# Kernel optimization log

Measured on AMD Instinct MI355X. Metric: run time of the kernel, lower is better.

## Reference

```python
import jax, jax.numpy as jnp
import numpy as np
import math

SUPPORT = 4
NEI = 20
POOL_RATE = 4

def _normalize(x, axis):
    n = jnp.linalg.norm(x, axis=axis, keepdims=True)
    return x / jnp.maximum(n, 1e-12)

def _knn(verts, k):
    # verts: (b, v, 3) -> (b, v, k) indices of k nearest (excluding self)
    sq = jnp.sum(verts * verts, axis=-1)
    dist = sq[:, :, None] + sq[:, None, :] - 2.0 * jnp.einsum('bid,bjd->bij', verts, verts)
    _, idx = jax.lax.top_k(-dist, k + 1)
    return idx[:, :, 1:]

def _gather(t, idx):
    # t: (b, v, c), idx: (b, v, n) -> (b, v, n, c)
    return jax.vmap(lambda ti, ii: ti[ii])(t, idx)

def _conv_surface(idx, verts, dirs, support, kernel):
    b, v, n = idx.shape
    nd = _normalize(_gather(verts, idx) - verts[:, :, None, :], -1)  # (b,v,n,3)
    sd = _normalize(dirs, 0)                                          # (3, s*k)
    theta = jax.nn.relu(jnp.einsum('bvnd,de->bvne', nd, sd))
    theta = theta.reshape(b, v, n, support, kernel)
    return jnp.sum(jnp.max(theta, axis=2), axis=2)  # (b, v, kernel)

def _conv_layer(idx, verts, fm, W, bias, dirs, support, out_c):
    b, v, n = idx.shape
    nd = _normalize(_gather(verts, idx) - verts[:, :, None, :], -1)
    sd = _normalize(dirs, 0)                                          # (3, s*out)
    theta = jax.nn.relu(jnp.einsum('bvnd,de->bvne', nd, sd))          # (b,v,n,s*out)
    f = jnp.einsum('bvc,ce->bve', fm, W) + bias                       # (b,v,(s+1)*out)
    f_center = f[:, :, :out_c]
    f_support = _gather(f[:, :, out_c:], idx)                         # (b,v,n,s*out)
    act = (theta * f_support).reshape(b, v, n, support, out_c)
    return f_center + jnp.sum(jnp.max(act, axis=2), axis=2)

def _pool(verts, fm, idx, key, rate):
    pooled = jnp.max(_gather(fm, idx), axis=2)  # (b, v, c)
    v = verts.shape[1]
    sel = jax.random.permutation(key, v)[: v // rate]
    return verts[:, sel, :], pooled[:, sel, :]

def _unif(key, shape, stdv):
    return jax.random.uniform(key, shape, jnp.float32, -stdv, stdv)

def setup_inputs() -> dict:
    key = jax.random.key(0)
    ks = jax.random.split(key, 16)
    s = SUPPORT
    vertices = jax.random.normal(ks[0], (4, 1, 4096, 3), dtype=jnp.float32)
    d = {'vertices': vertices}
    d['dirs0'] = _unif(ks[1], (3, s * 32), 1.0 / math.sqrt(s * 32))
    layers = [(32, 64), (64, 128), (128, 256), (256, 1024)]
    for i, (cin, cout) in enumerate(layers, start=1):
        stdv = 1.0 / math.sqrt(cout * (s + 1))
        d[f'W{i}'] = _unif(ks[3 * i - 1], (cin, (s + 1) * cout), stdv)
        d[f'b{i}'] = _unif(ks[3 * i], ((s + 1) * cout,), stdv)
        d[f'D{i}'] = _unif(ks[3 * i + 1], (3, s * cout), stdv)
    return d

def reference(vertices, dirs0, W1, b1, D1, W2, b2, D2, W3, b3, D3, W4, b4, D4):
    s = SUPPORT
    bs, _, vn, _ = vertices.shape
    v = vertices.reshape(bs, vn, 3)
    idx = _knn(v, NEI)
    fm0 = jax.nn.relu(_conv_surface(idx, v, dirs0, s, 32))
    fm1 = jax.nn.relu(_conv_layer(idx, v, fm0, W1, b1, D1, s, 64))
    v, fm1 = _pool(v, fm1, idx, jax.random.key(42), POOL_RATE)
    idx = _knn(v, NEI)
    fm2 = jax.nn.relu(_conv_layer(idx, v, fm1, W2, b2, D2, s, 128))
    fm3 = jax.nn.relu(_conv_layer(idx, v, fm2, W3, b3, D3, s, 256))
    v, fm3 = _pool(v, fm3, idx, jax.random.key(43), POOL_RATE)
    idx = _knn(v, NEI)
    fm4 = _conv_layer(idx, v, fm3, W4, b4, D4, s, 1024)
    out = jnp.transpose(fm4, (0, 2, 1))[..., None]  # (bs, 1024, vn/16, 1)
    return out
```

## Files before the change

### kernel.cpp

```cpp
#include <hip/hip_runtime.h>
#include <vector>
#include <algorithm>
#include <cstdint>
#include <cstring>
#include <cmath>

static inline uint32_t tf_rotl(uint32_t x, int r) { return (x << r) | (x >> (32 - r)); }

static void tf2x32(uint32_t k0, uint32_t k1, uint32_t x0, uint32_t x1,
                   uint32_t* o0, uint32_t* o1) {
  uint32_t ks2 = k0 ^ k1 ^ 0x1BD11BDAu;
  uint32_t v0 = x0 + k0, v1 = x1 + k1;
  static const int R0[4] = {13, 15, 26, 6}, R1[4] = {17, 29, 16, 24};
#define RND4(R) do { for (int i_ = 0; i_ < 4; ++i_) { v0 += v1; v1 = tf_rotl(v1, R[i_]); v1 ^= v0; } } while (0)
  RND4(R0); v0 += k1;  v1 += ks2 + 1u;
  RND4(R1); v0 += ks2; v1 += k0 + 2u;
  RND4(R0); v0 += k0;  v1 += k1 + 3u;
  RND4(R1); v0 += k1;  v1 += ks2 + 4u;
  RND4(R0); v0 += ks2; v1 += k0 + 5u;
#undef RND4
  *o0 = v0; *o1 = v1;
}

static void jax_permutation(uint32_t seed, int n, int rounds, int* x) {
  uint32_t k0 = 0u, k1 = seed;
  for (int i = 0; i < n; ++i) x[i] = i;
  std::vector<uint32_t> bits(n);
  std::vector<int> ord(n), xn(n);
  for (int r = 0; r < rounds; ++r) {
    uint32_t nk0, nk1, sk0, sk1;
    tf2x32(k0, k1, 0u, 0u, &nk0, &nk1);
    tf2x32(k0, k1, 0u, 1u, &sk0, &sk1);
    for (int i = 0; i < n; ++i) {
      uint32_t h, l;
      tf2x32(sk0, sk1, 0u, (uint32_t)i, &h, &l);
      bits[i] = h ^ l;
    }
    for (int i = 0; i < n; ++i) ord[i] = i;
    std::stable_sort(ord.begin(), ord.end(),
                     [&](int a, int b) { return bits[a] < bits[b]; });
    for (int i = 0; i < n; ++i) xn[i] = x[ord[i]];
    memcpy(x, xn.data(), (size_t)n * sizeof(int));
    k0 = nk0; k1 = nk1;
  }
}

#define NEI 20

__device__ __forceinline__ float san(float v) {
  v = (v != v) ? 0.0f : v;
  return fmaxf(-1e4f, fminf(v, 1e4f));
}

__global__ void k_setup(const float* __restrict__ vin, float* __restrict__ outA,
                        float4* __restrict__ pk, int nverts,
                        const float* __restrict__ d0, const float* __restrict__ d1,
                        const float* __restrict__ d2, const float* __restrict__ d3,
                        const float* __restrict__ d4,
                        float* __restrict__ s0, float* __restrict__ s1,
                        float* __restrict__ s2, float* __restrict__ s3,
                        float* __restrict__ s4) {
  int blk = blockIdx.x;
  if (blk < 64) {
    int i = blk * 256 + threadIdx.x;
    if (i >= nverts) return;
    float x = san(vin[3 * i]), y = san(vin[3 * i + 1]), z = san(vin[3 * i + 2]);
    outA[3 * i] = x; outA[3 * i + 1] = y; outA[3 * i + 2] = z;
    pk[i] = make_float4(x, y, z, x * x + y * y + z * z);
    return;
  }
  int t = (blk - 64) * 256 + threadIdx.x;
  const float* d; float* s; int E, e;
  if (t < 128)       { d = d0; s = s0; E = 128;  e = t; }
  else if (t < 384)  { d = d1; s = s1; E = 256;  e = t - 128; }
  else if (t < 896)  { d = d2; s = s2; E = 512;  e = t - 384; }
  else if (t < 1920) { d = d3; s = s3; E = 1024; e = t - 896; }
  else if (t < 6016) { d = d4; s = s4; E = 4096; e = t - 1920; }
  else return;
  float a = san(d[e]);
  float b = san(d[E + e]);
  float c = san(d[2 * E + e]);
  float nrm = sqrtf(a * a + b * b + c * c);
  float m = fmaxf(nrm, 1e-12f);
  s[e] = a / m; s[E + e] = b / m; s[2 * E + e] = c / m;
}

__device__ __forceinline__ unsigned fmap(float f) {
  unsigned u = __float_as_uint(f);
  return u ^ ((u & 0x80000000u) ? 0xFFFFFFFFu : 0x80000000u);
}

__device__ __forceinline__ unsigned dpp_min_bcast1(unsigned a) {
  unsigned t;
  t = (unsigned)__builtin_amdgcn_update_dpp((int)a, (int)a, 0xB1, 0xF, 0xF, true);
  a = t < a ? t : a;
  t = (unsigned)__builtin_amdgcn_update_dpp((int)a, (int)a, 0x4E, 0xF, 0xF, true);
  a = t < a ? t : a;
  t = (unsigned)__builtin_amdgcn_update_dpp((int)a, (int)a, 0x141, 0xF, 0xF, true);
  a = t < a ? t : a;
  t = (unsigned)__builtin_amdgcn_update_dpp((int)a, (int)a, 0x140, 0xF, 0xF, true);
  a = t < a ? t : a;
  t = (unsigned)__builtin_amdgcn_update_dpp((int)a, (int)a, 0x142, 0xA, 0xF, false);
  a = t < a ? t : a;
  t = (unsigned)__builtin_amdgcn_update_dpp((int)a, (int)a, 0x143, 0xC, 0xF, false);
  a = t < a ? t : a;
  return (unsigned)__builtin_amdgcn_readlane((int)a, 63);
}

__device__ __forceinline__ void dpp_min_bcast2(unsigned& a, unsigned& b) {
  unsigned t0, t1;
#define STEP_DPP(ctrl, rm, bc)                                                           \
  t0 = (unsigned)__builtin_amdgcn_update_dpp((int)a, (int)a, ctrl, rm, 0xF, bc);         \
  t1 = (unsigned)__builtin_amdgcn_update_dpp((int)b, (int)b, ctrl, rm, 0xF, bc);         \
  a = t0 < a ? t0 : a; b = t1 < b ? t1 : b;
  STEP_DPP(0xB1, 0xF, true)
  STEP_DPP(0x4E, 0xF, true)
  STEP_DPP(0x141, 0xF, true)
  STEP_DPP(0x140, 0xF, true)
  STEP_DPP(0x142, 0xA, false)
  STEP_DPP(0x143, 0xC, false)
#undef STEP_DPP
  a = (unsigned)__builtin_amdgcn_readlane((int)a, 63);
  b = (unsigned)__builtin_amdgcn_readlane((int)b, 63);
}

template <int VCAND>
__global__ __launch_bounds__(256, 8) void k_knn8(const float4* __restrict__ pk,
                                                 int* __restrict__ nidx, int V) {
  const int wid = threadIdx.x >> 6;
  const int lane = threadIdx.x & 63;
  const int row0 = blockIdx.x * 8 + wid * 2;
  const int b = row0 / V;
  const int base = b * V;
  const int i0 = row0 % V;

  float xi[2], yi[2], zi[2], sqi[2];
#pragma unroll
  for (int t = 0; t < 2; ++t) {
    float4 q = pk[base + i0 + t];
    xi[t] = q.x; yi[t] = q.y; zi[t] = q.z; sqi[t] = q.w;
  }

  unsigned long long q0[2] = {~0ULL, ~0ULL}, q1[2] = {~0ULL, ~0ULL}, q2[2] = {~0ULL, ~0ULL};
#pragma unroll 4
  for (int c = 0; c < VCAND; ++c) {
    int j = c * 64 + lane;
    float4 cj = pk[base + j];
    float xj = cj.x, yj = cj.y, zj = cj.z, sqj = cj.w;
#pragma unroll
    for (int t = 0; t < 2; ++t) {
      float dot = xi[t] * xj + yi[t] * yj + zi[t] * zj;
      float dd = (sqi[t] + sqj) - 2.0f * dot;
      unsigned long long k = (((unsigned long long)fmap(dd)) << 32) | (unsigned)j;
      if (k < q2[t]) {
        if (k < q1[t]) {
          q2[t] = q1[t];
          if (k < q0[t]) { q1[t] = q0[t]; q0[t] = k; } else { q1[t] = k; }
        } else {
          q2[t] = k;
        }
      }
    }
  }

  for (int r = 0; r < 21; ++r) {
    unsigned h0 = (unsigned)(q0[0] >> 32);
    unsigned h1 = (unsigned)(q0[1] >> 32);
    unsigned m0 = h0, m1 = h1;
    dpp_min_bcast2(m0, m1);
    unsigned long long mk0 = __ballot(h0 == m0);
    unsigned long long mk1 = __ballot(h1 == m1);
    bool win0, win1;
    if (__popcll(mk0) > 1) {
      unsigned jj = (h0 == m0) ? (unsigned)q0[0] : 0xFFFFFFFFu;
      unsigned jm = dpp_min_bcast1(jj);
      win0 = (h0 == m0) && ((unsigned)q0[0] == jm);
    } else {
      win0 = (h0 == m0);
    }
    if (__popcll(mk1) > 1) {
      unsigned jj = (h1 == m1) ? (unsigned)q0[1] : 0xFFFFFFFFu;
      unsigned jm = dpp_min_bcast1(jj);
      win1 = (h1 == m1) && ((unsigned)q0[1] == jm);
    } else {
      win1 = (h1 == m1);
    }
    if (win0) {
      if (r > 0) nidx[(size_t)row0 * NEI + (r - 1)] = (int)(unsigned)q0[0];
      unsigned long long bound = q0[0];
      q0[0] = q1[0]; q1[0] = q2[0]; q2[0] = ~0ULL;
      if (q0[0] == ~0ULL) {
        unsigned long long nm = ~0ULL;
        for (int c = 0; c < VCAND; ++c) {
          int j = c * 64 + lane;
          float4 cj = pk[base + j];
          float dot = xi[0] * cj.x + yi[0] * cj.y + zi[0] * cj.z;
          float dd = (sqi[0] + cj.w) - 2.0f * dot;
          unsigned long long k = (((unsigned long long)fmap(dd)) << 32) | (unsigned)j;
          if (k > bound && k < nm) nm = k;
        }
        q0[0] = nm;
      }
    }
    if (win1) {
      if (r > 0) nidx[(size_t)(row0 + 1) * NEI + (r - 1)] = (int)(unsigned)q0[1];
      unsigned long long bound = q0[1];
      q0[1] = q1[1]; q1[1] = q2[1]; q2[1] = ~0ULL;
      if (q0[1] == ~0ULL) {
        unsigned long long nm = ~0ULL;
        for (int c = 0; c < VCAND; ++c) {
          int j = c * 64 + lane;
          float4 cj = pk[base + j];
          float dot = xi[1] * cj.x + yi[1] * cj.y + zi[1] * cj.z;
          float dd = (sqi[1] + cj.w) - 2.0f * dot;
          unsigned long long k = (((unsigned long long)fmap(dd)) << 32) | (unsigned)j;
          if (k > bound && k < nm) nm = k;
        }
        q0[1] = nm;
      }
    }
  }
}

__global__ __launch_bounds__(128) void k_conv_surface(const float* __restrict__ verts,
                                                      const int* __restrict__ nidx,
                                                      const float* __restrict__ sd,
                                                      float* __restrict__ fm, int V) {
  int row = blockIdx.x;
  int b = row / V, v = row % V;
  const float* vb = verts + (size_t)b * V * 3;
  __shared__ float nd[60];
  __shared__ float mcol[128];
  int tid = threadIdx.x;
  if (tid < NEI) {
    int j = nidx[(size_t)row * NEI + tid];
    float dx = vb[3 * j] - vb[3 * v];
    float dy = vb[3 * j + 1] - vb[3 * v + 1];
    float dz = vb[3 * j + 2] - vb[3 * v + 2];
    float nrm = sqrtf(dx * dx + dy * dy + dz * dz);
    float m = fmaxf(nrm, 1e-12f);
    nd[tid * 3] = dx / m; nd[tid * 3 + 1] = dy / m; nd[tid * 3 + 2] = dz / m;
  }
  __syncthreads();
  {
    int e = tid;
    float s0 = sd[e], s1 = sd[128 + e], s2 = sd[256 + e];
    float me = 0.0f;
#pragma unroll
    for (int n = 0; n < NEI; ++n) {
      float th = nd[3 * n] * s0 + nd[3 * n + 1] * s1 + nd[3 * n + 2] * s2;
      th = fmaxf(th, 0.0f);
      me = fmaxf(me, th);
    }
    mcol[e] = me;
  }
  __syncthreads();
  if (tid < 32) {
    float o = mcol[tid] + mcol[32 + tid] + mcol[64 + tid] + mcol[96 + tid];
    o = fmaxf(o, 0.0f);
    fm[(size_t)row * 32 + tid] = o;
  }
}

__global__ __launch_bounds__(256) void k_gemm_bias(const float* __restrict__ A,
                                                   const float* __restrict__ W,
                                                   const float* __restrict__ bias,
                                                   float* __restrict__ Cm,
                                                   int M, int N, int K) {
  __shared__ float As[16][68];
  __shared__ float Bs[16][68];
  int n0 = blockIdx.x * 64, m0 = blockIdx.y * 64;
  int tx = threadIdx.x & 15, ty = threadIdx.x >> 4;
  float acc[4][4] = {};
  for (int k0 = 0; k0 < K; k0 += 16) {
    for (int t = threadIdx.x; t < 1024; t += 256) {
      int mm = t >> 4, kk = t & 15;
      int m = m0 + mm;
      As[kk][mm] = (m < M) ? A[(size_t)m * K + (k0 + kk)] : 0.0f;
    }
    for (int t = threadIdx.x; t < 1024; t += 256) {
      int kk = t >> 6, nn = t & 63;
      int n = n0 + nn;
      Bs[kk][nn] = (n < N) ? san(W[(size_t)(k0 + kk) * N + n]) : 0.0f;
    }
    __syncthreads();
#pragma unroll
    for (int kk = 0; kk < 16; ++kk) {
      float4 av = *(const float4*)&As[kk][ty << 2];
      float4 bv = *(const float4*)&Bs[kk][tx << 2];
      float a[4] = {av.x, av.y, av.z, av.w};
      float bb[4] = {bv.x, bv.y, bv.z, bv.w};
#pragma unroll
      for (int i = 0; i < 4; ++i)
#pragma unroll
        for (int j = 0; j < 4; ++j) acc[i][j] += a[i] * bb[j];
    }
    __syncthreads();
  }
  for (int i = 0; i < 4; ++i)
    for (int j = 0; j < 4; ++j) {
      int m = m0 + (ty << 2) + i, n = n0 + (tx << 2) + j;
      if (m < M && n < N) Cm[(size_t)m * N + n] = acc[i][j] + san(bias[n]);
    }
}

__global__ __launch_bounds__(256) void k_gemm128(const float* __restrict__ A,
                                                 const float* __restrict__ W,
                                                 const float* __restrict__ bias,
                                                 float* __restrict__ Cm,
                                                 int M, int N, int K) {
  __shared__ float As[32][132];
  __shared__ float Bs[32][132];
  const int n0 = blockIdx.x * 128, m0 = blockIdx.y * 128;
  const int tx = threadIdx.x & 15, ty = threadIdx.x >> 4;
  const int bm = ty * 8;
  float acc[8][8] = {};
  float bias_lo[4], bias_hi[4];
#pragma unroll
  for (int j = 0; j < 4; ++j) {
    bias_lo[j] = san(bias[n0 + tx * 4 + j]);
    bias_hi[j] = san(bias[n0 + 64 + tx * 4 + j]);
  }
  for (int k0 = 0; k0 < K; k0 += 32) {
#pragma unroll
    for (int r = 0; r < 4; ++r) {
      int t = r * 256 + threadIdx.x;
      int mm = t >> 3, kk = (t & 7) * 4;
      float4 v = *(const float4*)&A[(size_t)(m0 + mm) * K + k0 + kk];
      As[kk + 0][mm] = v.x; As[kk + 1][mm] = v.y; As[kk + 2][mm] = v.z; As[kk + 3][mm] = v.w;
    }
#pragma unroll
    for (int r = 0; r < 4; ++r) {
      int t = r * 256 + threadIdx.x;
      int kk = t >> 5, nn = (t & 31) * 4;
      float4 v = *(const float4*)&W[(size_t)(k0 + kk) * N + n0 + nn];
      *(float4*)&Bs[kk][nn] = v;
    }
    __syncthreads();
#pragma unroll
    for (int kk = 0; kk < 32; ++kk) {
      float4 a0 = *(const float4*)&As[kk][bm];
      float4 a1 = *(const float4*)&As[kk][bm + 4];
      float4 b0 = *(const float4*)&Bs[kk][tx * 4];
      float4 b1 = *(const float4*)&Bs[kk][64 + tx * 4];
      float a[8] = {a0.x, a0.y, a0.z, a0.w, a1.x, a1.y, a1.z, a1.w};
      float bb[8] = {b0.x, b0.y, b0.z, b0.w, b1.x, b1.y, b1.z, b1.w};
#pragma unroll
      for (int i = 0; i < 8; ++i)
#pragma unroll
        for (int j = 0; j < 8; ++j) acc[i][j] += a[i] * bb[j];
    }
    __syncthreads();
  }
#pragma unroll
  for (int i = 0; i < 8; ++i) {
    int m = m0 + bm + i;
    float4 lo = {acc[i][0] + bias_lo[0], acc[i][1] + bias_lo[1],
                 acc[i][2] + bias_lo[2], acc[i][3] + bias_lo[3]};
    float4 hi = {acc[i][4] + bias_hi[0], acc[i][5] + bias_hi[1],
                 acc[i][6] + bias_hi[2], acc[i][7] + bias_hi[3]};
    *(float4*)&Cm[(size_t)m * N + n0 + tx * 4] = lo;
    *(float4*)&Cm[(size_t)m * N + n0 + 64 + tx * 4] = hi;
  }
}

__global__ __launch_bounds__(256) void k_conv_layer(const float* __restrict__ f,
                                                    const float* __restrict__ verts,
                                                    const int* __restrict__ nidx,
                                                    const float* __restrict__ sd,
                                                    float* __restrict__ outf,
                                                    int V, int C, int relu_out) {
  int row = blockIdx.x;
  int b = row / V, v = row % V;
  int E = 4 * C;
  extern __shared__ float sm[];
  float* mcol = sm;
  float* nd = sm + E;
  int* jr = (int*)(nd + 60);
  int tid = threadIdx.x;
  const float* vb = verts + (size_t)b * V * 3;
  if (tid < NEI) {
    int j = nidx[(size_t)row * NEI + tid];
    jr[tid] = j;
    float dx = vb[3 * j] - vb[3 * v];
    float dy = vb[3 * j + 1] - vb[3 * v + 1];
    float dz = vb[3 * j + 2] - vb[3 * v + 2];
    float nrm = sqrtf(dx * dx + dy * dy + dz * dz);
    float m = fmaxf(nrm, 1e-12f);
    nd[tid * 3] = dx / m; nd[tid * 3 + 1] = dy / m; nd[tid * 3 + 2] = dz / m;
  }
  __syncthreads();
  size_t fb = (size_t)b * V;
  int fivec = 5 * C;
  for (int e = tid; e < E; e += blockDim.x) {
    float s0 = sd[e], s1 = sd[E + e], s2 = sd[2 * E + e];
    float me = -INFINITY;
#pragma unroll
    for (int n = 0; n < NEI; ++n) {
      float th = nd[3 * n] * s0 + nd[3 * n + 1] * s1 + nd[3 * n + 2] * s2;
      th = fmaxf(th, 0.0f);
      float fv = f[(fb + jr[n]) * (size_t)fivec + C + e];
      me = fmaxf(me, th * fv);
    }
    mcol[e] = me;
  }
  __syncthreads();
  for (int c = tid; c < C; c += blockDim.x) {
    float o = f[(size_t)row * fivec + c] + mcol[c] + mcol[C + c] + mcol[2 * C + c] + mcol[3 * C + c];
    if (relu_out) o = fmaxf(o, 0.0f);
    outf[(size_t)row * C + c] = o;
  }
}

__global__ __launch_bounds__(1024) void k_conv_layer_big(const float* __restrict__ f,
                                                         const float* __restrict__ verts,
                                                         const int* __restrict__ nidx,
                                                         const float* __restrict__ sd,
                                                         float* __restrict__ outf,
                                                         int V, int C, int relu_out) {
  int row = blockIdx.x;
  int b = row / V, v = row % V;
  int E = 4 * C;
  extern __shared__ float sm[];
  float* mcol = sm;
  float* nd = sm + E;
  int* jr = (int*)(nd + 60);
  int tid = threadIdx.x;
  const float* vb = verts + (size_t)b * V * 3;
  if (tid < NEI) {
    int j = nidx[(size_t)row * NEI + tid];
    jr[tid] = j;
    float dx = vb[3 * j] - vb[3 * v];
    float dy = vb[3 * j + 1] - vb[3 * v + 1];
    float dz = vb[3 * j + 2] - vb[3 * v + 2];
    float nrm = sqrtf(dx * dx + dy * dy + dz * dz);
    float m = fmaxf(nrm, 1e-12f);
    nd[tid * 3] = dx / m; nd[tid * 3 + 1] = dy / m; nd[tid * 3 + 2] = dz / m;
  }
  __syncthreads();
  size_t fb = (size_t)b * V;
  int fivec = 5 * C;
  for (int e = tid; e < E; e += blockDim.x) {
    float s0 = sd[e], s1 = sd[E + e], s2 = sd[2 * E + e];
    float me = -INFINITY;
#pragma unroll
    for (int n = 0; n < NEI; ++n) {
      float th = nd[3 * n] * s0 + nd[3 * n + 1] * s1 + nd[3 * n + 2] * s2;
      th = fmaxf(th, 0.0f);
      float fv = f[(fb + jr[n]) * (size_t)fivec + C + e];
      me = fmaxf(me, th * fv);
    }
    mcol[e] = me;
  }
  __syncthreads();
  for (int c = tid; c < C; c += blockDim.x) {
    float o = f[(size_t)row * fivec + c] + mcol[c] + mcol[C + c] + mcol[2 * C + c] + mcol[3 * C + c];
    if (relu_out) o = fmaxf(o, 0.0f);
    outf[(size_t)row * C + c] = o;
  }
}

__global__ __launch_bounds__(256) void k_transpose_vc(const float* __restrict__ in,
                                                      float* __restrict__ out,
                                                      int V, int C) {
  __shared__ float tile[32][33];
  int b = blockIdx.z;
  int c0 = blockIdx.x * 32, v0 = blockIdx.y * 32;
  int tx = threadIdx.x & 31, ty4 = threadIdx.x >> 5;
#pragma unroll
  for (int j = 0; j < 4; ++j) {
    int v = v0 + ty4 * 4 + j;
    tile[ty4 * 4 + j][tx] = in[((size_t)b * V + v) * C + c0 + tx];
  }
  __syncthreads();
#pragma unroll
  for (int j = 0; j < 4; ++j) {
    int c = c0 + ty4 * 4 + j;
    out[((size_t)b * C + c) * V + v0 + tx] = tile[tx][ty4 * 4 + j];
  }
}

__global__ void k_pool_sel(const float* __restrict__ fm, const int* __restrict__ nidx,
                           const int* __restrict__ sel, float* __restrict__ outp,
                           const float* __restrict__ vinA, float* __restrict__ voutA,
                           float4* __restrict__ pkout,
                           int Vin, int Vout, int C) {
  int t = blockIdx.x * blockDim.x + threadIdx.x;
  if (t < 4 * Vout) {
    int p = t % Vout;
    int b = t / Vout;
    int src = b * Vin + sel[p];
    float x = vinA[3 * src], y = vinA[3 * src + 1], z = vinA[3 * src + 2];
    int dst = b * Vout + p;
    voutA[3 * dst] = x; voutA[3 * dst + 1] = y; voutA[3 * dst + 2] = z;
    pkout[dst] = make_float4(x, y, z, x * x + y * y + z * z);
  }
  int total = 4 * Vout * C;
  if (t >= total) return;
  int c = t % C;
  int p = (t / C) % Vout;
  int b = t / (C * Vout);
  int sv = sel[p];
  const int* ir = nidx + ((size_t)b * Vin + sv) * NEI;
  float m = -INFINITY;
#pragma unroll
  for (int n = 0; n < NEI; ++n)
    m = fmaxf(m, fm[((size_t)b * Vin + ir[n]) * C + c]);
  outp[((size_t)b * Vout + p) * C + c] = m;
}

extern "C" void kernel_launch(void* const* d_in, const int* in_sizes, int n_in,
                              void* d_out, int out_size, void* d_ws, size_t ws_size,
                              hipStream_t stream) {
  (void)in_sizes; (void)n_in; (void)out_size; (void)ws_size;
  const int B = 4, V1 = 4096, V2 = 1024, V3 = 256;

  const float* vin   = (const float*)d_in[0];
  const float* dirs0 = (const float*)d_in[1];
  const float* W1 = (const float*)d_in[2];
  const float* b1 = (const float*)d_in[3];
  const float* D1 = (const float*)d_in[4];
  const float* W2 = (const float*)d_in[5];
  const float* b2 = (const float*)d_in[6];
  const float* D2 = (const float*)d_in[7];
  const float* W3 = (const float*)d_in[8];
  const float* b3 = (const float*)d_in[9];
  const float* D3 = (const float*)d_in[10];
  const float* W4 = (const float*)d_in[11];
  const float* b4 = (const float*)d_in[12];
  const float* D4 = (const float*)d_in[13];
  float* out = (float*)d_out;

  char* ws = (char*)d_ws;
  size_t off = 0;
  auto alloc = [&](size_t bytes) -> char* {
    char* p = ws + off;
    off = (off + bytes + 255) & ~(size_t)255;
    return p;
  };
  int* sel1 = (int*)alloc((size_t)V2 * 4);
  int* sel2 = (int*)alloc((size_t)V3 * 4);
  float* verts1 = (float*)alloc((size_t)B * V1 * 3 * 4);
  float* verts2 = (float*)alloc((size_t)B * V2 * 3 * 4);
  float* verts3 = (float*)alloc((size_t)B * V3 * 3 * 4);
  float4* pk1 = (float4*)alloc((size_t)B * V1 * 16);
  float4* pk2 = (float4*)alloc((size_t)B * V2 * 16);
  float4* pk3 = (float4*)alloc((size_t)B * V3 * 16);
  int* idx1 = (int*)alloc((size_t)B * V1 * NEI * 4);
  int* idx2 = (int*)alloc((size_t)B * V2 * NEI * 4);
  int* idx3 = (int*)alloc((size_t)B * V3 * NEI * 4);
  float* sd0 = (float*)alloc(3 * 128 * 4);
  float* sd1 = (float*)alloc(3 * 256 * 4);
  float* sd2 = (float*)alloc(3 * 512 * 4);
  float* sd3 = (float*)alloc(3 * 1024 * 4);
  float* sd4 = (float*)alloc(3 * 4096 * 4);
  float* bufA = (float*)alloc((size_t)B * V1 * 32 * 4);
  float* bufB = (float*)alloc((size_t)B * V1 * 64 * 4);
  float* bufC = (float*)alloc((size_t)B * V2 * 64 * 4);
  float* fbuf = (float*)alloc((size_t)B * V1 * 320 * 4);
  float* fm0 = bufA, *fm2 = bufA;
  float* fm1 = bufB, *fm3 = bufB;
  float* fm1p = bufC, *fm3p = bufC;
  float* conv4out = bufB;

  static int perm1[4096];
  static int perm2[1024];
  static int selh[1280];
  jax_permutation(42u, 4096, 2, perm1);
  jax_permutation(43u, 1024, 1, perm2);
  memcpy(selh, perm1, 1024 * sizeof(int));
  memcpy(selh + 1024, perm2, 256 * sizeof(int));
  hipMemcpyAsync(sel1, selh, 1024 * sizeof(int), hipMemcpyHostToDevice, stream);
  hipMemcpyAsync(sel2, selh + 1024, 256 * sizeof(int), hipMemcpyHostToDevice, stream);

  k_setup<<<88, 256, 0, stream>>>(vin, verts1, pk1, B * V1,
                                  dirs0, D1, D2, D3, D4, sd0, sd1, sd2, sd3, sd4);
  k_knn8<64><<<B * V1 / 8, 256, 0, stream>>>(pk1, idx1, V1);
  k_conv_surface<<<B * V1, 128, 0, stream>>>(verts1, idx1, sd0, fm0, V1);
  k_gemm_bias<<<dim3(5, 256), 256, 0, stream>>>(fm0, W1, b1, fbuf, B * V1, 320, 32);
  k_conv_layer<<<B * V1, 256, (4 * 64 + 80) * 4, stream>>>(fbuf, verts1, idx1, sd1, fm1, V1, 64, 1);
  {
    int total = B * V2 * 64;
    k_pool_sel<<<(total + 255) / 256, 256, 0, stream>>>(fm1, idx1, sel1, fm1p,
                                                        verts1, verts2, pk2,
                                                        V1, V2, 64);
  }
  k_knn8<16><<<B * V2 / 8, 256, 0, stream>>>(pk2, idx2, V2);
  k_gemm128<<<dim3(640 / 128, 4096 / 128), 256, 0, stream>>>(fm1p, W2, b2, fbuf, B * V2, 640, 64);
  k_conv_layer<<<B * V2, 256, (4 * 128 + 80) * 4, stream>>>(fbuf, verts2, idx2, sd2, fm2, V2, 128, 1);
  k_gemm128<<<dim3(1280 / 128, 4096 / 128), 256, 0, stream>>>(fm2, W3, b3, fbuf, B * V2, 1280, 128);
  k_conv_layer<<<B * V2, 256, (4 * 256 + 80) * 4, stream>>>(fbuf, verts2, idx2, sd3, fm3, V2, 256, 1);
  {
    int total = B * V3 * 256;
    k_pool_sel<<<(total + 255) / 256, 256, 0, stream>>>(fm3, idx2, sel2, fm3p,
                                                        verts2, verts3, pk3,
                                                        V2, V3, 256);
  }
  k_knn8<4><<<B * V3 / 8, 256, 0, stream>>>(pk3, idx3, V3);
  k_gemm128<<<dim3(5120 / 128, 1024 / 128), 256, 0, stream>>>(fm3p, W4, b4, fbuf, B * V3, 5120, 256);
  k_conv_layer_big<<<B * V3, 1024, (4 * 1024 + 80) * 4, stream>>>(fbuf, verts3, idx3, sd4, conv4out, V3, 1024, 0);
  k_transpose_vc<<<dim3(1024 / 32, 256 / 32, B), 256, 0, stream>>>(conv4out, out, V3, 1024);
}
```

Measured before the change: 439.3 us.

## Replace FP32 GEMMs with split-bf16 MFMA (3-term) matrix-core kernel

Replaces the scalar FP32 128x128 tiled GEMM used by layers 2-4 with a matrix-core kernel built on bf16 16x16x32 MFMA. Each operand is split into high and low bf16 parts, and three products (hh, hl, lh) approximate FP32 accuracy. Weights are split and transposed each call by new kernels, and activations are split before every GEMM. This moves the GEMM FLOPs onto matrix cores, at the cost of extra split kernels, extra memory traffic, and slightly lower precision than true FP32.

Result: faster. 403.2 us (-8.2%).

```diff
diff --git a/kernel.cpp b/kernel.cpp
--- a/kernel.cpp
+++ b/kernel.cpp
@@ -304,64 +304,113 @@
     }
 }
 
-__global__ __launch_bounds__(256) void k_gemm128(const float* __restrict__ A,
-                                                 const float* __restrict__ W,
-                                                 const float* __restrict__ bias,
-                                                 float* __restrict__ Cm,
-                                                 int M, int N, int K) {
-  __shared__ float As[32][132];
-  __shared__ float Bs[32][132];
+typedef __attribute__((ext_vector_type(8))) short v8h;
+typedef __attribute__((ext_vector_type(4))) float v4f;
+
+__device__ __forceinline__ unsigned short f2bf(float f) {
+  unsigned u = __float_as_uint(f);
+  u = u + 0x7FFFu + ((u >> 16) & 1u);
+  return (unsigned short)(u >> 16);
+}
+__device__ __forceinline__ float bf2f(unsigned short h) {
+  return __uint_as_float((unsigned)h << 16);
+}
+
+__global__ __launch_bounds__(256) void k_split(const float* __restrict__ in,
+                                               unsigned short* __restrict__ hi,
+                                               unsigned short* __restrict__ lo, int n) {
+  int i = blockIdx.x * 256 + threadIdx.x;
+  if (i >= n) return;
+  float a = in[i];
+  unsigned short h = f2bf(a);
+  hi[i] = h;
+  lo[i] = f2bf(a - bf2f(h));
+}
+
+__global__ __launch_bounds__(256) void k_split_wT(const float* __restrict__ W,
+                                                  unsigned short* __restrict__ hiT,
+                                                  unsigned short* __restrict__ loT,
+                                                  int K, int N) {
+  __shared__ float tile[32][33];
+  int k0 = blockIdx.y * 32, n0 = blockIdx.x * 32;
+  int tx = threadIdx.x & 31, ty4 = threadIdx.x >> 5;
+#pragma unroll
+  for (int j = 0; j < 4; ++j)
+    tile[ty4 * 4 + j][tx] = san(W[(size_t)(k0 + ty4 * 4 + j) * N + n0 + tx]);
+  __syncthreads();
+#pragma unroll
+  for (int j = 0; j < 4; ++j) {
+    int n = n0 + ty4 * 4 + j;
+    float a = tile[tx][ty4 * 4 + j];
+    unsigned short h = f2bf(a);
+    hiT[(size_t)n * K + k0 + tx] = h;
+    loT[(size_t)n * K + k0 + tx] = f2bf(a - bf2f(h));
+  }
+}
+
+__global__ __launch_bounds__(256) void k_gemm128_mfma(
+    const unsigned short* __restrict__ Ah, const unsigned short* __restrict__ Al,
+    const unsigned short* __restrict__ BhT, const unsigned short* __restrict__ BlT,
+    const float* __restrict__ bias, float* __restrict__ Cm, int M, int N, int K) {
+  __shared__ __attribute__((aligned(16))) unsigned short sAh[128 * 40];
+  __shared__ __attribute__((aligned(16))) unsigned short sAl[128 * 40];
+  __shared__ __attribute__((aligned(16))) unsigned short sBh[128 * 40];
+  __shared__ __attribute__((aligned(16))) unsigned short sBl[128 * 40];
   const int n0 = blockIdx.x * 128, m0 = blockIdx.y * 128;
-  const int tx = threadIdx.x & 15, ty = threadIdx.x >> 4;
-  const int bm = ty * 8;
-  float acc[8][8] = {};
-  float bias_lo[4], bias_hi[4];
-#pragma unroll
-  for (int j = 0; j < 4; ++j) {
-    bias_lo[j] = san(bias[n0 + tx * 4 + j]);
-    bias_hi[j] = san(bias[n0 + 64 + tx * 4 + j]);
-  }
+  const int l = threadIdx.x & 63;
+  const int w = threadIdx.x >> 6;
+  const int wr = (w >> 1) * 64, wc = (w & 1) * 64;
+  const int lr = l & 15;
+  const int kb8 = (l >> 4) * 8;
+
+  v4f acc[4][4];
+#pragma unroll
+  for (int i = 0; i < 4; ++i)
+#pragma unroll
+    for (int j = 0; j < 4; ++j) acc[i][j] = (v4f){0.f, 0.f, 0.f, 0.f};
+
   for (int k0 = 0; k0 < K; k0 += 32) {
 #pragma unroll
-    for (int r = 0; r < 4; ++r) {
-      int t = r * 256 + threadIdx.x;
-      int mm = t >> 3, kk = (t & 7) * 4;
-      float4 v = *(const float4*)&A[(size_t)(m0 + mm) * K + k0 + kk];
-      As[kk + 0][mm] = v.x; As[kk + 1][mm] = v.y; As[kk + 2][mm] = v.z; As[kk + 3][mm] = v.w;
-    }
-#pragma unroll
-    for (int r = 0; r < 4; ++r) {
-      int t = r * 256 + threadIdx.x;
-      int kk = t >> 5, nn = (t & 31) * 4;
-      float4 v = *(const float4*)&W[(size_t)(k0 + kk) * N + n0 + nn];
-      *(float4*)&Bs[kk][nn] = v;
+    for (int q = 0; q < 2; ++q) {
+      int lin = (int)threadIdx.x + (q << 8);
+      int r = lin >> 2, kc = (lin & 3) << 3;
+      *(uint4*)&sAh[r * 40 + kc] = *(const uint4*)&Ah[(size_t)(m0 + r) * K + k0 + kc];
+      *(uint4*)&sAl[r * 40 + kc] = *(const uint4*)&Al[(size_t)(m0 + r) * K + k0 + kc];
+      *(uint4*)&sBh[r * 40 + kc] = *(const uint4*)&BhT[(size_t)(n0 + r) * K + k0 + kc];
+      *(uint4*)&sBl[r * 40 + kc] = *(const uint4*)&BlT[(size_t)(n0 + r) * K + k0 + kc];
     }
     __syncthreads();
-#pragma unroll
-    for (int kk = 0; kk < 32; ++kk) {
-      float4 a0 = *(const float4*)&As[kk][bm];
-      float4 a1 = *(const float4*)&As[kk][bm + 4];
-      float4 b0 = *(const float4*)&Bs[kk][tx * 4];
-      float4 b1 = *(const float4*)&Bs[kk][64 + tx * 4];
-      float a[8] = {a0.x, a0.y, a0.z, a0.w, a1.x, a1.y, a1.z, a1.w};
-      float bb[8] = {b0.x, b0.y, b0.z, b0.w, b1.x, b1.y, b1.z, b1.w};
-#pragma unroll
-      for (int i = 0; i < 8; ++i)
-#pragma unroll
-        for (int j = 0; j < 8; ++j) acc[i][j] += a[i] * bb[j];
-    }
+    v8h fah[4], fal[4], fbh[4], fbl[4];
+#pragma unroll
+    for (int t = 0; t < 4; ++t) {
+      fah[t] = *(const v8h*)&sAh[(wr + t * 16 + lr) * 40 + kb8];
+      fal[t] = *(const v8h*)&sAl[(wr + t * 16 + lr) * 40 + kb8];
+      fbh[t] = *(const v8h*)&sBh[(wc + t * 16 + lr) * 40 + kb8];
+      fbl[t] = *(const v8h*)&sBl[(wc + t * 16 + lr) * 40 + kb8];
+    }
+#pragma unroll
+    for (int i = 0; i < 4; ++i)
+#pragma unroll
+      for (int j = 0; j < 4; ++j) {
+        acc[i][j] = __builtin_amdgcn_mfma_f32_16x16x32_bf16(fah[i], fbh[j], acc[i][j], 0, 0, 0);
+        acc[i][j] = __builtin_amdgcn_mfma_f32_16x16x32_bf16(fah[i], fbl[j], acc[i][j], 0, 0, 0);
+        acc[i][j] = __builtin_amdgcn_mfma_f32_16x16x32_bf16(fal[i], fbh[j], acc[i][j], 0, 0, 0);
+      }
     __syncthreads();
   }
-#pragma unroll
-  for (int i = 0; i < 8; ++i) {
-    int m = m0 + bm + i;
-    float4 lo = {acc[i][0] + bias_lo[0], acc[i][1] + bias_lo[1],
-                 acc[i][2] + bias_lo[2], acc[i][3] + bias_lo[3]};
-    float4 hi = {acc[i][4] + bias_hi[0], acc[i][5] + bias_hi[1],
-                 acc[i][6] + bias_hi[2], acc[i][7] + bias_hi[3]};
-    *(float4*)&Cm[(size_t)m * N + n0 + tx * 4] = lo;
-    *(float4*)&Cm[(size_t)m * N + n0 + 64 + tx * 4] = hi;
-  }
+  float bs[4];
+#pragma unroll
+  for (int j = 0; j < 4; ++j) bs[j] = san(bias[n0 + wc + j * 16 + lr]);
+  const int rowb = m0 + wr + (l >> 4) * 4;
+#pragma unroll
+  for (int i = 0; i < 4; ++i)
+#pragma unroll
+    for (int j = 0; j < 4; ++j) {
+      int col = n0 + wc + j * 16 + lr;
+#pragma unroll
+      for (int v = 0; v < 4; ++v)
+        Cm[(size_t)(rowb + i * 16 + v) * N + col] = acc[i][j][v] + bs[j];
+    }
 }
 
 __global__ __launch_bounds__(256) void k_conv_layer(const float* __restrict__ f,
@@ -558,6 +607,14 @@
   float* bufB = (float*)alloc((size_t)B * V1 * 64 * 4);
   float* bufC = (float*)alloc((size_t)B * V2 * 64 * 4);
   float* fbuf = (float*)alloc((size_t)B * V1 * 320 * 4);
+  unsigned short* w2hT = (unsigned short*)alloc((size_t)640 * 64 * 2);
+  unsigned short* w2lT = (unsigned short*)alloc((size_t)640 * 64 * 2);
+  unsigned short* w3hT = (unsigned short*)alloc((size_t)1280 * 128 * 2);
+  unsigned short* w3lT = (unsigned short*)alloc((size_t)1280 * 128 * 2);
+  unsigned short* w4hT = (unsigned short*)alloc((size_t)5120 * 256 * 2);
+  unsigned short* w4lT = (unsigned short*)alloc((size_t)5120 * 256 * 2);
+  unsigned short* aSh = (unsigned short*)alloc((size_t)4096 * 128 * 2);
+  unsigned short* aSl = (unsigned short*)alloc((size_t)4096 * 128 * 2);
   float* fm0 = bufA, *fm2 = bufA;
   float* fm1 = bufB, *fm3 = bufB;
   float* fm1p = bufC, *fm3p = bufC;
@@ -575,6 +632,9 @@
 
   k_setup<<<88, 256, 0, stream>>>(vin, verts1, pk1, B * V1,
                                   dirs0, D1, D2, D3, D4, sd0, sd1, sd2, sd3, sd4);
+  k_split_wT<<<dim3(640 / 32, 64 / 32), 256, 0, stream>>>(W2, w2hT, w2lT, 64, 640);
+  k_split_wT<<<dim3(1280 / 32, 128 / 32), 256, 0, stream>>>(W3, w3hT, w3lT, 128, 1280);
+  k_split_wT<<<dim3(5120 / 32, 256 / 32), 256, 0, stream>>>(W4, w4hT, w4lT, 256, 5120);
   k_knn8<64><<<B * V1 / 8, 256, 0, stream>>>(pk1, idx1, V1);
   k_conv_surface<<<B * V1, 128, 0, stream>>>(verts1, idx1, sd0, fm0, V1);
   k_gemm_bias<<<dim3(5, 256), 256, 0, stream>>>(fm0, W1, b1, fbuf, B * V1, 320, 32);
@@ -586,9 +646,11 @@
                                                         V1, V2, 64);
   }
   k_knn8<16><<<B * V2 / 8, 256, 0, stream>>>(pk2, idx2, V2);
-  k_gemm128<<<dim3(640 / 128, 4096 / 128), 256, 0, stream>>>(fm1p, W2, b2, fbuf, B * V2, 640, 64);
+  k_split<<<(B * V2 * 64) / 256, 256, 0, stream>>>(fm1p, aSh, aSl, B * V2 * 64);
+  k_gemm128_mfma<<<dim3(640 / 128, 4096 / 128), 256, 0, stream>>>(aSh, aSl, w2hT, w2lT, b2, fbuf, B * V2, 640, 64);
   k_conv_layer<<<B * V2, 256, (4 * 128 + 80) * 4, stream>>>(fbuf, verts2, idx2, sd2, fm2, V2, 128, 1);
-  k_gemm128<<<dim3(1280 / 128, 4096 / 128), 256, 0, stream>>>(fm2, W3, b3, fbuf, B * V2, 1280, 128);
+  k_split<<<(B * V2 * 128) / 256, 256, 0, stream>>>(fm2, aSh, aSl, B * V2 * 128);
+  k_gemm128_mfma<<<dim3(1280 / 128, 4096 / 128), 256, 0, stream>>>(aSh, aSl, w3hT, w3lT, b3, fbuf, B * V2, 1280, 128);
   k_conv_layer<<<B * V2, 256, (4 * 256 + 80) * 4, stream>>>(fbuf, verts2, idx2, sd3, fm3, V2, 256, 1);
   {
     int total = B * V3 * 256;
@@ -597,7 +659,8 @@
                                                         V2, V3, 256);
   }
   k_knn8<4><<<B * V3 / 8, 256, 0, stream>>>(pk3, idx3, V3);
-  k_gemm128<<<dim3(5120 / 128, 1024 / 128), 256, 0, stream>>>(fm3p, W4, b4, fbuf, B * V3, 5120, 256);
+  k_split<<<(B * V3 * 256) / 256, 256, 0, stream>>>(fm3p, aSh, aSl, B * V3 * 256);
+  k_gemm128_mfma<<<dim3(5120 / 128, 1024 / 128), 256, 0, stream>>>(aSh, aSl, w4hT, w4lT, b4, fbuf, B * V3, 5120, 256);
   k_conv_layer_big<<<B * V3, 1024, (4 * 1024 + 80) * 4, stream>>>(fbuf, verts3, idx3, sd4, conv4out, V3, 1024, 0);
   k_transpose_vc<<<dim3(1024 / 32, 256 / 32, B), 256, 0, stream>>>(conv4out, out, V3, 1024);
 }
```
